# Kernel optimization log

Hardware: AMD Instinct MI355X
Metric: run time of the kernel (lower is better)

## Reference

```python
import jax, jax.numpy as jnp
import numpy as np

N_NODES = 100000
N_EDGES = 3200000
IN_CH = 128
HID = 32


def setup_inputs() -> dict:
    key = jax.random.key(0)
    k1, k2, k3, k4 = jax.random.split(key, 4)
    x = jax.random.normal(k1, (N_NODES, IN_CH), dtype=jnp.float32)
    edge_index = jax.random.randint(k2, (2, N_EDGES), 0, N_NODES, dtype=jnp.int64)
    # Glorot-style scale for weights
    W1 = jax.random.normal(k3, (IN_CH, HID), dtype=jnp.float32) * (1.0 / np.sqrt(IN_CH))
    b1 = jnp.zeros((HID,), dtype=jnp.float32)
    W2 = jax.random.normal(k4, (HID, HID), dtype=jnp.float32) * (1.0 / np.sqrt(HID))
    b2 = jnp.zeros((HID,), dtype=jnp.float32)
    return {"x": x, "edge_index": edge_index, "W1": W1, "b1": b1, "W2": W2, "b2": b2}


def _gcn_conv(x, src, dst, norm, W, b, n_nodes):
    # PyG GCNConv: h = x @ W, then symmetric-normalized scatter-add, then + bias
    h = x @ W                                   # [N, out]
    msg = h[src] * norm[:, None]                # gather + per-edge scale
    out = jax.ops.segment_sum(msg, dst, num_segments=n_nodes)  # scatter-add
    return out + b


def reference(x, edge_index, W1, b1, W2, b2):
    n = x.shape[0]
    loop = jnp.arange(n, dtype=edge_index.dtype)
    # add self-loops (PyG default add_self_loops=True)
    src = jnp.concatenate([edge_index[0], loop])
    dst = jnp.concatenate([edge_index[1], loop])
    # symmetric normalization deg^-1/2 on destination-side in-degree (incl. self-loops)
    deg = jax.ops.segment_sum(jnp.ones_like(dst, dtype=x.dtype), dst, num_segments=n)
    dinv = jnp.where(deg > 0, jax.lax.rsqrt(deg), 0.0)
    norm = dinv[src] * dinv[dst]                # [E + N]
    h = _gcn_conv(x, src, dst, norm, W1, b1, n)
    h = jax.nn.relu(h)
    out = _gcn_conv(h, src, dst, norm, W2, b2, n)
    return out
```

## Files before the change

kernel.cpp:

```cpp
#include <hip/hip_runtime.h>
#include <hip/hip_bf16.h>

#define N_NODES 100000
#define N_EDGES 3200000
#define IN_CH   128
#define HID     32
#define NB      1024
#define NPB     98
#define CAP     4096
#define CHUNK   4096
#define ACC_LD  33
#define NPASS   8
#define OCTN    12500u
#define FXS     1048576.0f
#define FXI     (1.0f/1048576.0f)
#define NTILE   6250
#define TPW     2

__device__ __forceinline__ unsigned int pack_bf16x2(float a, float b) {
    unsigned int ua = __float_as_uint(a);
    unsigned int ub = __float_as_uint(b);
    ua = (ua + 0x7FFFu + ((ua >> 16) & 1u)) >> 16;
    ub = (ub + 0x7FFFu + ((ub >> 16) & 1u)) >> 16;
    return (ua & 0xFFFFu) | (ub << 16);
}
__device__ __forceinline__ float bf_lo(unsigned int v) { return __uint_as_float(v << 16); }
__device__ __forceinline__ float bf_hi(unsigned int v) { return __uint_as_float(v & 0xFFFF0000u); }
__device__ __forceinline__ int   f2fx(float f)         { return (int)(f * FXS); }
__device__ __forceinline__ float hif(float f) {
    return __uint_as_float(__float_as_uint(f) & 0xFFFF0000u);
}
__device__ __forceinline__ unsigned int tpack(float a, float b) {
    return (__float_as_uint(a) >> 16) | (__float_as_uint(b) & 0xFFFF0000u);
}
__device__ __forceinline__ unsigned short bf16_rne(float f) {
    unsigned int u = __float_as_uint(f);
    return (unsigned short)((u + 0x7FFFu + ((u >> 16) & 1u)) >> 16);
}

typedef short bf16x8 __attribute__((ext_vector_type(8)));
typedef float f32x4  __attribute__((ext_vector_type(4)));
union frag_u { bf16x8 f; unsigned int u[4]; };

__global__ __launch_bounds__(256) void detect_idx(const int* __restrict__ ei,
                                                  int* __restrict__ flag) {
    __shared__ int nz;
    if (threadIdx.x == 0) nz = 0;
    __syncthreads();
    if (ei[2 * threadIdx.x + 1] != 0) atomicAdd(&nz, 1);
    __syncthreads();
    if (threadIdx.x == 0) flag[0] = (nz == 0) ? 1 : 0;
}

__device__ __forceinline__ int edge_at(const int* __restrict__ ei, int idx64,
                                       size_t pos) {
    if (idx64) return (int)((const long long*)ei)[pos];
    return ei[pos];
}

__global__ __launch_bounds__(256) void bcur_init(int* __restrict__ bcur) {
    int b = blockIdx.x * 256 + threadIdx.x;
    if (b < NB) bcur[b] = b * CAP;
}

__global__ __launch_bounds__(256) void bucket_scatter3(
    const int* __restrict__ ei,
    const int* __restrict__ flag,
    int* __restrict__ bcur,
    unsigned int* __restrict__ ebuf) {
    __shared__ int cnt[NB];
    __shared__ int base_l[NB];

    int t = threadIdx.x;
    for (int j = t; j < NB; j += 256) cnt[j] = 0;
    __syncthreads();

    int e0 = blockIdx.x * CHUNK;
    int nE = N_EDGES - e0; if (nE > CHUNK) nE = CHUNK;
    int idx64 = flag[0];

    for (int i = t; i < nE; i += 256) {
        unsigned int d = (unsigned int)edge_at(ei, idx64, (size_t)N_EDGES + e0 + i);
        atomicAdd(&cnt[d / NPB], 1);
    }
    __syncthreads();

    for (int j = t; j < NB; j += 256) {
        int c = cnt[j];
        base_l[j] = (c > 0) ? atomicAdd(&bcur[j], c) : 0;
        cnt[j] = 0;
    }
    __syncthreads();

    for (int i = t; i < nE; i += 256) {
        unsigned int s = (unsigned int)edge_at(ei, idx64, (size_t)(e0 + i));
        unsigned int d = (unsigned int)edge_at(ei, idx64, (size_t)N_EDGES + e0 + i);
        unsigned int b = d / NPB;
        int p = atomicAdd(&cnt[b], 1);
        ebuf[base_l[b] + p] = (s << 8) | (d - b * NPB);
    }
}

__global__ __launch_bounds__(256) void finalize_csr(
    const int* __restrict__ bcur,
    unsigned int* __restrict__ ebuf,
    float* __restrict__ dinv,
    int* __restrict__ octp) {
    __shared__ unsigned int lbuf[CAP];
    __shared__ unsigned int sbuf[CAP];
    __shared__ int lhist[NPB];
    __shared__ int oh[8];
    __shared__ int obase[9];
    __shared__ int ocur[8];
    int b = blockIdx.x, t = threadIdx.x;
    int n0 = b * NPB;
    int nn = N_NODES - n0; if (nn > NPB) nn = NPB; if (nn < 0) nn = 0;
    int cnt = bcur[b] - b * CAP;
    unsigned int* reg = ebuf + (size_t)b * CAP;

    for (int j = t; j < NPB; j += 256) lhist[j] = 0;
    if (t < 8) oh[t] = 0;
    __syncthreads();

    for (int i = t; i < cnt; i += 256) {
        unsigned int e = reg[i];
        lbuf[i] = e;
        atomicAdd(&lhist[e & 255u], 1);
        atomicAdd(&oh[(e >> 8) / OCTN], 1);
    }
    __syncthreads();

    for (int j = t; j < nn; j += 256)
        dinv[n0 + j] = rsqrtf((float)(lhist[j] + 1));

    if (t == 0) {
        obase[0] = 0;
        for (int p = 0; p < 8; ++p) {
            obase[p + 1] = obase[p] + oh[p];
            ocur[p] = obase[p];
        }
    }
    __syncthreads();

    for (int i = t; i < cnt; i += 256) {
        unsigned int e = lbuf[i];
        int p = (int)((e >> 8) / OCTN);
        int pos = atomicAdd(&ocur[p], 1);
        sbuf[pos] = e;
    }
    __syncthreads();

    for (int i = t; i < cnt; i += 256)
        reg[i] = sbuf[i];
    if (t < 9) octp[b * 9 + t] = obase[t];
}

__global__ __launch_bounds__(256) void gemm1_mfma(
    const float* __restrict__ x,
    const float* __restrict__ W1,
    const float* __restrict__ dinv,
    unsigned short* __restrict__ h1u) {
    int wv   = blockIdx.x * 4 + (threadIdx.x >> 6);
    int lane = threadIdx.x & 63;
    int lq   = lane & 15;
    int kh   = lane >> 4;

    frag_u bh[2][4], bl[2][4];
#pragma unroll
    for (int t = 0; t < 2; ++t) {
#pragma unroll
        for (int s = 0; s < 4; ++s) {
            int ch = t * 16 + lq;
            int k0 = s * 32 + kh * 8;
            float w[8], wh[8];
#pragma unroll
            for (int i = 0; i < 8; ++i) {
                w[i]  = W1[(k0 + i) * HID + ch];
                wh[i] = hif(w[i]);
            }
#pragma unroll
            for (int j = 0; j < 4; ++j) {
                bh[t][s].u[j] = tpack(wh[2 * j], wh[2 * j + 1]);
                bl[t][s].u[j] = tpack(w[2 * j] - wh[2 * j],
                                      w[2 * j + 1] - wh[2 * j + 1]);
            }
        }
    }

#pragma unroll 1
    for (int it = 0; it < TPW; ++it) {
        int tile = wv * TPW + it;
        if (tile >= NTILE) return;
        int n0 = tile * 16;
        const float* xr = x + (size_t)(n0 + lq) * IN_CH;

        f32x4 acc0 = {0.f, 0.f, 0.f, 0.f};
        f32x4 acc1 = {0.f, 0.f, 0.f, 0.f};
#pragma unroll
        for (int s = 0; s < 4; ++s) {
            int k0 = s * 32 + kh * 8;
            float4 v0 = *reinterpret_cast<const float4*>(xr + k0);
            float4 v1 = *reinterpret_cast<const float4*>(xr + k0 + 4);
            frag_u ah, al;
            ah.u[0] = tpack(v0.x, v0.y);
            ah.u[1] = tpack(v0.z, v0.w);
            ah.u[2] = tpack(v1.x, v1.y);
            ah.u[3] = tpack(v1.z, v1.w);
            al.u[0] = tpack(v0.x - hif(v0.x), v0.y - hif(v0.y));
            al.u[1] = tpack(v0.z - hif(v0.z), v0.w - hif(v0.w));
            al.u[2] = tpack(v1.x - hif(v1.x), v1.y - hif(v1.y));
            al.u[3] = tpack(v1.z - hif(v1.z), v1.w - hif(v1.w));

            acc0 = __builtin_amdgcn_mfma_f32_16x16x32_bf16(ah.f, bh[0][s].f, acc0, 0, 0, 0);
            acc0 = __builtin_amdgcn_mfma_f32_16x16x32_bf16(al.f, bh[0][s].f, acc0, 0, 0, 0);
            acc0 = __builtin_amdgcn_mfma_f32_16x16x32_bf16(ah.f, bl[0][s].f, acc0, 0, 0, 0);
            acc1 = __builtin_amdgcn_mfma_f32_16x16x32_bf16(ah.f, bh[1][s].f, acc1, 0, 0, 0);
            acc1 = __builtin_amdgcn_mfma_f32_16x16x32_bf16(al.f, bh[1][s].f, acc1, 0, 0, 0);
            acc1 = __builtin_amdgcn_mfma_f32_16x16x32_bf16(ah.f, bl[1][s].f, acc1, 0, 0, 0);
        }

#pragma unroll
        for (int j = 0; j < 4; ++j) {
            int node = n0 + kh * 4 + j;
            float dn = dinv[node];
            unsigned short* dst = h1u + (size_t)node * 32 + lq;
            dst[0]  = bf16_rne(acc0[j] * dn);
            dst[16] = bf16_rne(acc1[j] * dn);
        }
    }
}

__device__ __forceinline__ uint4 row_q(const unsigned int* __restrict__ hb,
                                       unsigned int s, int q4) {
    return *reinterpret_cast<const uint4*>(hb + (size_t)s * 16 + q4);
}

__device__ __forceinline__ void fx_scatter8(int* acc, unsigned int e,
                                            int co, uint4 v) {
    int* a = acc + (int)(e & 255u) * ACC_LD + co;
    atomicAdd(&a[0], f2fx(bf_lo(v.x))); atomicAdd(&a[1], f2fx(bf_hi(v.x)));
    atomicAdd(&a[2], f2fx(bf_lo(v.y))); atomicAdd(&a[3], f2fx(bf_hi(v.y)));
    atomicAdd(&a[4], f2fx(bf_lo(v.z))); atomicAdd(&a[5], f2fx(bf_hi(v.z)));
    atomicAdd(&a[6], f2fx(bf_lo(v.w))); atomicAdd(&a[7], f2fx(bf_hi(v.w)));
}

__global__ __launch_bounds__(512, 8) void agg1_srt(
    const int* __restrict__ bcur,
    const unsigned int* __restrict__ ebuf,
    const int* __restrict__ octp,
    const unsigned int* __restrict__ h1b,
    const float* __restrict__ dinv,
    const float* __restrict__ b1,
    const float* __restrict__ W2,
    unsigned int* __restrict__ h3b) {
    __shared__ int acc[NPB * ACC_LD];
    __shared__ float w2s[HID * HID];
    __shared__ float b1s[HID];
    int b = blockIdx.x, t = threadIdx.x;
    int n0 = b * NPB;
    int nn = N_NODES - n0; if (nn > NPB) nn = NPB; if (nn < 0) nn = 0;
    const unsigned int* reg = ebuf + (size_t)b * CAP;

    for (int i = t; i < HID * HID; i += 512) w2s[i] = W2[i];
    if (t < HID) b1s[t] = b1[t];

    for (int u = t; u < nn * 4; u += 512) {
        int n = u >> 2, q = u & 3;
        uint4 sv = *reinterpret_cast<const uint4*>(h1b + (size_t)(n0 + n) * 16 + 4 * q);
        int* a = &acc[n * ACC_LD + 8 * q];
        a[0] = f2fx(bf_lo(sv.x)); a[1] = f2fx(bf_hi(sv.x));
        a[2] = f2fx(bf_lo(sv.y)); a[3] = f2fx(bf_hi(sv.y));
        a[4] = f2fx(bf_lo(sv.z)); a[5] = f2fx(bf_hi(sv.z));
        a[6] = f2fx(bf_lo(sv.w)); a[7] = f2fx(bf_hi(sv.w));
    }
    __syncthreads();

    int q4 = (t & 3) * 4;
    int co = (t & 3) * 8;
#pragma unroll 1
    for (int p = 0; p < NPASS; ++p) {
        int o1 = octp[b * 9 + p + 1];
        int i  = octp[b * 9 + p] + (t >> 2);
        for (; i + 128 < o1; i += 256) {
            unsigned int e0 = reg[i];
            unsigned int e1 = reg[i + 128];
            uint4 v0 = row_q(h1b, e0 >> 8, q4);
            uint4 v1 = row_q(h1b, e1 >> 8, q4);
            fx_scatter8(acc, e0, co, v0);
            fx_scatter8(acc, e1, co, v1);
        }
        if (i < o1) {
            unsigned int e = reg[i];
            uint4 v = row_q(h1b, e >> 8, q4);
            fx_scatter8(acc, e, co, v);
        }
    }
    __syncthreads();

    float* h2s = (float*)acc;
    for (int u = t; u < nn * HID; u += 512) {
        int n = u >> 5, j = u & 31;
        float v = (float)acc[n * ACC_LD + j] * FXI * dinv[n0 + n] + b1s[j];
        h2s[n * ACC_LD + j] = v > 0.f ? v : 0.f;
    }
    __syncthreads();

    for (int u = t; u < nn * 4; u += 512) {
        int n = u >> 2, qq = u & 3;
        const float* h2 = &h2s[n * ACC_LD];
        float a2[8];
#pragma unroll
        for (int k = 0; k < 8; ++k) a2[k] = 0.f;
#pragma unroll
        for (int j = 0; j < HID; ++j) {
            float hj = h2[j];
            const float* wr = &w2s[j * HID + 8 * qq];
#pragma unroll
            for (int k = 0; k < 8; ++k) a2[k] += hj * wr[k];
        }
        float dn = dinv[n0 + n];
        unsigned int* dst = h3b + (size_t)(n0 + n) * 16 + 4 * qq;
        *reinterpret_cast<uint4*>(dst) = make_uint4(
            pack_bf16x2(a2[0] * dn, a2[1] * dn),
            pack_bf16x2(a2[2] * dn, a2[3] * dn),
            pack_bf16x2(a2[4] * dn, a2[5] * dn),
            pack_bf16x2(a2[6] * dn, a2[7] * dn));
    }
}

__global__ __launch_bounds__(512, 8) void agg2_srt(
    const int* __restrict__ bcur,
    const unsigned int* __restrict__ ebuf,
    const int* __restrict__ octp,
    const unsigned int* __restrict__ h3b,
    const float* __restrict__ dinv,
    const float* __restrict__ b2,
    float* __restrict__ out) {
    __shared__ int acc[NPB * ACC_LD];
    __shared__ float b2s[HID];
    int b = blockIdx.x, t = threadIdx.x;
    int n0 = b * NPB;
    int nn = N_NODES - n0; if (nn > NPB) nn = NPB; if (nn < 0) nn = 0;
    const unsigned int* reg = ebuf + (size_t)b * CAP;

    if (t < HID) b2s[t] = b2[t];

    for (int u = t; u < nn * 4; u += 512) {
        int n = u >> 2, q = u & 3;
        uint4 sv = *reinterpret_cast<const uint4*>(h3b + (size_t)(n0 + n) * 16 + 4 * q);
        int* a = &acc[n * ACC_LD + 8 * q];
        a[0] = f2fx(bf_lo(sv.x)); a[1] = f2fx(bf_hi(sv.x));
        a[2] = f2fx(bf_lo(sv.y)); a[3] = f2fx(bf_hi(sv.y));
        a[4] = f2fx(bf_lo(sv.z)); a[5] = f2fx(bf_hi(sv.z));
        a[6] = f2fx(bf_lo(sv.w)); a[7] = f2fx(bf_hi(sv.w));
    }
    __syncthreads();

    int q4 = (t & 3) * 4;
    int co = (t & 3) * 8;
#pragma unroll 1
    for (int p = 0; p < NPASS; ++p) {
        int o1 = octp[b * 9 + p + 1];
        int i  = octp[b * 9 + p] + (t >> 2);
        for (; i + 128 < o1; i += 256) {
            unsigned int e0 = reg[i];
            unsigned int e1 = reg[i + 128];
            uint4 v0 = row_q(h3b, e0 >> 8, q4);
            uint4 v1 = row_q(h3b, e1 >> 8, q4);
            fx_scatter8(acc, e0, co, v0);
            fx_scatter8(acc, e1, co, v1);
        }
        if (i < o1) {
            unsigned int e = reg[i];
            uint4 v = row_q(h3b, e >> 8, q4);
            fx_scatter8(acc, e, co, v);
        }
    }
    __syncthreads();

    for (int u = t; u < nn * 4; u += 512) {
        int n = u >> 2, qq = u & 3;
        float dn = dinv[n0 + n];
        const int* a = &acc[n * ACC_LD + 8 * qq];
        const float* bb = &b2s[8 * qq];
        float4 o1v, o2v;
        o1v.x = (float)a[0] * FXI * dn + bb[0];
        o1v.y = (float)a[1] * FXI * dn + bb[1];
        o1v.z = (float)a[2] * FXI * dn + bb[2];
        o1v.w = (float)a[3] * FXI * dn + bb[3];
        o2v.x = (float)a[4] * FXI * dn + bb[4];
        o2v.y = (float)a[5] * FXI * dn + bb[5];
        o2v.z = (float)a[6] * FXI * dn + bb[6];
        o2v.w = (float)a[7] * FXI * dn + bb[7];
        float* op = out + (size_t)(n0 + n) * 32 + 8 * qq;
        *reinterpret_cast<float4*>(op)     = o1v;
        *reinterpret_cast<float4*>(op + 4) = o2v;
    }
}

extern "C" void kernel_launch(void* const* d_in, const int* in_sizes, int n_in,
                              void* d_out, int out_size, void* d_ws, size_t ws_size,
                              hipStream_t stream) {
    const float* x  = (const float*)d_in[0];
    const int*   ei = (const int*)d_in[1];
    const float* W1 = (const float*)d_in[2];
    const float* b1 = (const float*)d_in[3];
    const float* W2 = (const float*)d_in[4];
    const float* b2 = (const float*)d_in[5];
    float* out = (float*)d_out;

    int*          flag = (int*)d_ws;
    int*          bcur = flag + 64;
    int*          octp = bcur + NB;
    float*        dinv = (float*)(octp + NB * 9);
    unsigned int* ebuf = (unsigned int*)(dinv + N_NODES);
    unsigned int* h1b  = ebuf + (size_t)NB * CAP;
    unsigned int* h3b  = h1b + (size_t)N_NODES * 16;

    const int chunkBlocks = (N_EDGES + CHUNK - 1) / CHUNK;
    const int g1Blocks    = (NTILE + 4 * TPW - 1) / (4 * TPW);

    detect_idx<<<1, 256, 0, stream>>>(ei, flag);

    bcur_init<<<(NB + 255) / 256, 256, 0, stream>>>(bcur);
    bucket_scatter3<<<chunkBlocks, 256, 0, stream>>>(ei, flag, bcur, ebuf);
    finalize_csr<<<NB, 256, 0, stream>>>(bcur, ebuf, dinv, octp);

    gemm1_mfma<<<g1Blocks, 256, 0, stream>>>(x, W1, dinv,
                                             (unsigned short*)h1b);
    agg1_srt<<<NB, 512, 0, stream>>>(bcur, ebuf, octp, h1b, dinv, b1, W2, h3b);

    agg2_srt<<<NB, 512, 0, stream>>>(bcur, ebuf, octp, h3b, dinv, b2, out);
}
```

Before: 247.4 us.

## Stage bucket scatter in shared memory for coalesced global writes

The edge bucketing kernel now computes a block-local prefix sum of bucket counts, sorts each chunk's packed edges into shared memory by bucket, and then writes them to global memory in sorted order, so consecutive threads write contiguous runs within each bucket. The chunk size doubles to 8192 edges with 512 threads per block, which halves the number of global atomics per bucket. This targets the scattered, uncoalesced global stores of the previous version. It costs about 60KB of shared memory per block, which lowers occupancy, and adds a serial scan with many barriers.

```diff
diff --git a/kernel.cpp b/kernel.cpp
--- a/kernel.cpp
+++ b/kernel.cpp
@@ -8,7 +8,7 @@
 #define NB      1024
 #define NPB     98
 #define CAP     4096
-#define CHUNK   4096
+#define CHUNK   8192
 #define ACC_LD  33
 #define NPASS   8
 #define OCTN    12500u
@@ -63,42 +63,68 @@
     if (b < NB) bcur[b] = b * CAP;
 }
 
-__global__ __launch_bounds__(256) void bucket_scatter3(
+__global__ __launch_bounds__(512) void bucket_scatter4(
     const int* __restrict__ ei,
     const int* __restrict__ flag,
     int* __restrict__ bcur,
     unsigned int* __restrict__ ebuf) {
     __shared__ int cnt[NB];
-    __shared__ int base_l[NB];
+    __shared__ int loff[NB];
+    __shared__ int dlt[NB];
+    __shared__ int tmp[512];
+    __shared__ unsigned int   sbuf[CHUNK];
+    __shared__ unsigned short sbb[CHUNK];
 
     int t = threadIdx.x;
-    for (int j = t; j < NB; j += 256) cnt[j] = 0;
+    for (int j = t; j < NB; j += 512) cnt[j] = 0;
     __syncthreads();
 
     int e0 = blockIdx.x * CHUNK;
     int nE = N_EDGES - e0; if (nE > CHUNK) nE = CHUNK;
     int idx64 = flag[0];
 
-    for (int i = t; i < nE; i += 256) {
+    for (int i = t; i < nE; i += 512) {
         unsigned int d = (unsigned int)edge_at(ei, idx64, (size_t)N_EDGES + e0 + i);
         atomicAdd(&cnt[d / NPB], 1);
     }
     __syncthreads();
 
-    for (int j = t; j < NB; j += 256) {
+    int c0 = cnt[2 * t], c1 = cnt[2 * t + 1];
+    int s = c0 + c1;
+    tmp[t] = s;
+    __syncthreads();
+    for (int off = 1; off < 512; off <<= 1) {
+        int x = 0;
+        if (t >= off) x = tmp[t - off];
+        __syncthreads();
+        if (t >= off) tmp[t] += x;
+        __syncthreads();
+    }
+    int base = tmp[t] - s;
+    loff[2 * t]     = base;
+    loff[2 * t + 1] = base + c0;
+    __syncthreads();
+
+    for (int j = t; j < NB; j += 512) {
         int c = cnt[j];
-        base_l[j] = (c > 0) ? atomicAdd(&bcur[j], c) : 0;
+        int gb = (c > 0) ? atomicAdd(&bcur[j], c) : 0;
+        dlt[j] = gb - loff[j];
         cnt[j] = 0;
     }
     __syncthreads();
 
-    for (int i = t; i < nE; i += 256) {
-        unsigned int s = (unsigned int)edge_at(ei, idx64, (size_t)(e0 + i));
-        unsigned int d = (unsigned int)edge_at(ei, idx64, (size_t)N_EDGES + e0 + i);
-        unsigned int b = d / NPB;
-        int p = atomicAdd(&cnt[b], 1);
-        ebuf[base_l[b] + p] = (s << 8) | (d - b * NPB);
-    }
+    for (int i = t; i < nE; i += 512) {
+        unsigned int sv = (unsigned int)edge_at(ei, idx64, (size_t)(e0 + i));
+        unsigned int d  = (unsigned int)edge_at(ei, idx64, (size_t)N_EDGES + e0 + i);
+        unsigned int b  = d / NPB;
+        int pos = loff[b] + atomicAdd(&cnt[b], 1);
+        sbuf[pos] = (sv << 8) | (d - b * NPB);
+        sbb[pos]  = (unsigned short)b;
+    }
+    __syncthreads();
+
+    for (int i = t; i < nE; i += 512)
+        ebuf[dlt[sbb[i]] + i] = sbuf[i];
 }
 
 __global__ __launch_bounds__(256) void finalize_csr(
@@ -423,7 +449,7 @@
     detect_idx<<<1, 256, 0, stream>>>(ei, flag);
 
     bcur_init<<<(NB + 255) / 256, 256, 0, stream>>>(bcur);
-    bucket_scatter3<<<chunkBlocks, 256, 0, stream>>>(ei, flag, bcur, ebuf);
+    bucket_scatter4<<<chunkBlocks, 512, 0, stream>>>(ei, flag, bcur, ebuf);
     finalize_csr<<<NB, 256, 0, stream>>>(bcur, ebuf, dinv, octp);
 
     gemm1_mfma<<<g1Blocks, 256, 0, stream>>>(x, W1, dinv,
```

Result: faster. 212.9 us (-13.9%).
